# Kernel tuning notes

Hardware: AMD Instinct MI355X
Metric: run time of the kernel (lower is better)

The kernel has to match this reference:

```python
import jax, jax.numpy as jnp
import numpy as np

B, S, D = 2, 2048, 1024
H = 16
HD = D // H  # 64


def setup_inputs() -> dict:
    key = jax.random.key(0)
    ks = jax.random.split(key, 9)
    s = 1.0 / np.sqrt(D)
    x = jax.random.normal(ks[0], (B, S, D), dtype=jnp.float32)
    Wq = jax.random.normal(ks[1], (D, D), dtype=jnp.float32) * s
    Wk = jax.random.normal(ks[2], (D, D), dtype=jnp.float32) * s
    Wv = jax.random.normal(ks[3], (D, D), dtype=jnp.float32) * s
    Wo = jax.random.normal(ks[4], (D, D), dtype=jnp.float32) * s
    bq = jnp.zeros((D,), jnp.float32)
    bk = jnp.zeros((D,), jnp.float32)
    bv = jnp.zeros((D,), jnp.float32)
    bo = jnp.zeros((D,), jnp.float32)
    # causal mask, broadcastable to (B, H, S, S)
    mask = jnp.tril(jnp.ones((S, S), dtype=bool))[None, None, :, :]
    return {"x": x, "Wq": Wq, "bq": bq, "Wk": Wk, "bk": bk,
            "Wv": Wv, "bv": bv, "Wo": Wo, "bo": bo, "mask": mask}


def _split_heads(t):
    # (B, S, D) -> (B, H, S, HD)
    b, s, _ = t.shape
    return t.reshape(b, s, H, HD).transpose(0, 2, 1, 3)


def reference(x, Wq, bq, Wk, bk, Wv, bv, Wo, bo, mask):
    q = _split_heads(x @ Wq + bq)
    k = _split_heads(x @ Wk + bk)
    v = _split_heads(x @ Wv + bv)
    scale = 1.0 / jnp.sqrt(jnp.asarray(HD, dtype=q.dtype))
    scores = jnp.einsum('bhqd,bhkd->bhqk', q, k) * scale
    large_neg = jnp.finfo(scores.dtype).min
    scores = jnp.where(mask, scores, large_neg)
    attn = jax.nn.softmax(scores, axis=-1)
    out = jnp.einsum('bhqk,bhkd->bhqd', attn, v)  # (B,H,S,HD)
    out = out.transpose(0, 2, 1, 3).reshape(x.shape[0], x.shape[1], D)
    return out @ Wo + bo
```

## Files before the change

kernel.cpp:

```cpp
#include <hip/hip_runtime.h>
#include <hip/hip_bf16.h>

typedef __attribute__((ext_vector_type(8))) short bf16x8;
typedef __attribute__((ext_vector_type(4))) float f32x4;

#define B_DIM  2
#define S_DIM  2048
#define D_DIM  1024
#define H_DIM  16
#define HD_DIM 64

__device__ __forceinline__ float bf2f(ushort u) {
    union { unsigned int ui; float f; } c; c.ui = ((unsigned int)u) << 16; return c.f;
}
__device__ __forceinline__ ushort f2bf(float f) {
    __hip_bfloat16 h = __float2bfloat16(f);
    return *reinterpret_cast<ushort*>(&h);
}

__device__ __forceinline__ void async_cp16(const ushort* g, ushort* l) {
    __builtin_amdgcn_global_load_lds(
        (const __attribute__((address_space(1))) void*)g,
        (__attribute__((address_space(3))) void*)l, 16, 0, 0);
}

__global__ __launch_bounds__(256) void detect_kernel(const ushort* __restrict__ x,
                                                     int* __restrict__ flag) {
    __shared__ int any;
    int tid = threadIdx.x;
    if (tid == 0) any = 0;
    __syncthreads();
    int cnt = 0;
    for (int j = 0; j < 64; ++j) {
        ushort u = x[tid * 64 + j];
        if (((u >> 7) & 0xFF) == 0xFF) cnt++;
    }
    if (cnt) atomicOr(&any, 1);
    __syncthreads();
    if (tid == 0) *flag = any ? 1 : 0;
}

__global__ __launch_bounds__(256) void prep_kernel(const void* __restrict__ x,
                                                   const void* __restrict__ Wq,
                                                   const void* __restrict__ Wk,
                                                   const void* __restrict__ Wv,
                                                   const void* __restrict__ Wo,
                                                   const void* __restrict__ bq,
                                                   const void* __restrict__ bk,
                                                   const void* __restrict__ bv,
                                                   const void* __restrict__ bo,
                                                   ushort* __restrict__ xc,
                                                   ushort* __restrict__ Wqkvt,
                                                   ushort* __restrict__ Wot,
                                                   float* __restrict__ biasf,
                                                   const int* __restrict__ flag) {
    int tid = threadIdx.x;
    int z = blockIdx.z;
    bool isf32 = (*flag != 0);

    if (z == 4) {
        int t = (blockIdx.y * 16 + blockIdx.x) * 256 + tid;
#pragma unroll
        for (int c = 0; c < 8; ++c) {
            int i = t + c * 65536;
            if (isf32) {
                const float* s = (const float*)x;
                f32x4 a = *(const f32x4*)&s[(size_t)i * 8];
                f32x4 b = *(const f32x4*)&s[(size_t)i * 8 + 4];
                bf16x8 o;
                o[0] = f2bf(a.x); o[1] = f2bf(a.y); o[2] = f2bf(a.z); o[3] = f2bf(a.w);
                o[4] = f2bf(b.x); o[5] = f2bf(b.y); o[6] = f2bf(b.z); o[7] = f2bf(b.w);
                *(bf16x8*)&xc[(size_t)i * 8] = o;
            } else {
                *(bf16x8*)&xc[(size_t)i * 8] =
                    *(const bf16x8*)&((const ushort*)x)[(size_t)i * 8];
            }
        }
        return;
    }
    if (z == 5) {
        int bid = blockIdx.y * 16 + blockIdx.x;
        if (bid >= 16) return;
        int i = bid * 256 + tid;
        int w = i >> 10, j = i & 1023;
        const void* s = (w == 0) ? bq : (w == 1) ? bk : (w == 2) ? bv : bo;
        biasf[i] = isf32 ? ((const float*)s)[j] : bf2f(((const ushort*)s)[j]);
        return;
    }

    __shared__ ushort tile[64][72];
    const void* src = (z == 0) ? Wq : (z == 1) ? Wk : (z == 2) ? Wv : Wo;
    ushort* dst = (z < 3) ? (Wqkvt + (size_t)z * D_DIM * D_DIM) : Wot;
    int r0 = blockIdx.y * 64, c0 = blockIdx.x * 64;
#pragma unroll
    for (int p = 0; p < 2; ++p) {
        int r = p * 32 + (tid >> 3);
        int c = (tid & 7) * 8;
        if (isf32) {
            const float* s = (const float*)src;
            f32x4 a = *(const f32x4*)&s[(size_t)(r0 + r) * D_DIM + c0 + c];
            f32x4 b = *(const f32x4*)&s[(size_t)(r0 + r) * D_DIM + c0 + c + 4];
            tile[r][c + 0] = f2bf(a.x); tile[r][c + 1] = f2bf(a.y);
            tile[r][c + 2] = f2bf(a.z); tile[r][c + 3] = f2bf(a.w);
            tile[r][c + 4] = f2bf(b.x); tile[r][c + 5] = f2bf(b.y);
            tile[r][c + 6] = f2bf(b.z); tile[r][c + 7] = f2bf(b.w);
        } else {
            *(bf16x8*)&tile[r][c] =
                *(const bf16x8*)&((const ushort*)src)[(size_t)(r0 + r) * D_DIM + c0 + c];
        }
    }
    __syncthreads();
#pragma unroll
    for (int p = 0; p < 2; ++p) {
        int n  = p * 32 + (tid >> 3);
        int cc = (tid & 7) * 8;
        bf16x8 v;
#pragma unroll
        for (int e = 0; e < 8; ++e) v[e] = (short)tile[cc + e][n];
        *(bf16x8*)&dst[(size_t)(c0 + n) * D_DIM + r0 + cc] = v;
    }
}

__global__ __launch_bounds__(256) void gemm128_kernel(const ushort* __restrict__ A,
                                                      const ushort* __restrict__ Bt,
                                                      const float* __restrict__ bias,
                                                      ushort* __restrict__ qkout,
                                                      ushort* __restrict__ vtout) {
    __shared__ ushort As[128 * 64];
    __shared__ ushort Bs[128 * 64];
    int tid  = threadIdx.x;
    int wave = tid >> 6;
    int lane = tid & 63;
    int l16  = lane & 15;
    int quad = lane >> 4;
    int m0   = blockIdx.y * 128;
    int n0   = blockIdx.x * 128;
    int wm   = wave >> 1;
    int wn   = wave & 1;
    const int K = 1024;

    f32x4 acc[4][4];
#pragma unroll
    for (int i = 0; i < 4; ++i)
#pragma unroll
        for (int j = 0; j < 4; ++j) acc[i][j] = (f32x4){0.f, 0.f, 0.f, 0.f};

    int lrow = lane >> 3;
    int gcol = ((lane & 7) ^ lrow) * 8;
    int sw   = l16 & 7;

    for (int kt = 0; kt < 16; ++kt) {
        int k0 = kt * 64;
#pragma unroll
        for (int j = 0; j < 4; ++j) {
            int chunk = wave * 4 + j;
            int grow  = chunk * 8 + lrow;
            async_cp16(&A[(size_t)(m0 + grow) * K + k0 + gcol], &As[chunk * 512]);
            async_cp16(&Bt[(size_t)(n0 + grow) * K + k0 + gcol], &Bs[chunk * 512]);
        }
        __syncthreads();

#pragma unroll
        for (int kb = 0; kb < 2; ++kb) {
            bf16x8 af[4], bf[4];
#pragma unroll
            for (int i = 0; i < 4; ++i)
                af[i] = *(const bf16x8*)&As[(wm * 64 + i * 16 + l16) * 64 +
                                            (((kb * 4 + quad) ^ sw) << 3)];
#pragma unroll
            for (int j = 0; j < 4; ++j)
                bf[j] = *(const bf16x8*)&Bs[(wn * 64 + j * 16 + l16) * 64 +
                                            (((kb * 4 + quad) ^ sw) << 3)];
#pragma unroll
            for (int i = 0; i < 4; ++i)
#pragma unroll
                for (int j = 0; j < 4; ++j)
                    acc[i][j] = __builtin_amdgcn_mfma_f32_16x16x32_bf16(af[i], bf[j],
                                                                        acc[i][j], 0, 0, 0);
        }
        __syncthreads();
    }

    const size_t TSZ = (size_t)B_DIM * H_DIM * S_DIM * HD_DIM;
#pragma unroll
    for (int j = 0; j < 4; ++j) {
        int n = n0 + wn * 64 + j * 16 + l16;
        float bv = bias[n];
        int which = n >> 10;
        int n1 = n & 1023;
        int h = n1 >> 6, hd = n1 & 63;
#pragma unroll
        for (int i = 0; i < 4; ++i) {
            int mb = m0 + wm * 64 + i * 16 + quad * 4;
            int b = mb >> 11, s = mb & (S_DIM - 1);
            float v4[4];
#pragma unroll
            for (int r = 0; r < 4; ++r) v4[r] = acc[i][j][r] + bv;
            if (which == 2) {
                ushort pk[4];
#pragma unroll
                for (int r = 0; r < 4; ++r) pk[r] = f2bf(v4[r]);
                *(uint2*)&vtout[(((size_t)(b * H_DIM + h) * HD_DIM + hd)) * S_DIM + s] =
                    *(uint2*)pk;
            } else {
#pragma unroll
                for (int r = 0; r < 4; ++r) {
                    float v = v4[r];
                    if (which == 0) v *= 0.18033688011f;
                    qkout[which * TSZ +
                          ((((size_t)(b * H_DIM + h)) * S_DIM + s + r) << 6) + hd] = f2bf(v);
                }
            }
        }
    }
}

__global__ __launch_bounds__(256) void gemm64_kernel(const ushort* __restrict__ A,
                                                     const ushort* __restrict__ Bt,
                                                     const float* __restrict__ bias,
                                                     void* __restrict__ out,
                                                     const int* __restrict__ flag) {
    __shared__ ushort As[64 * 64];
    __shared__ ushort Bs[128 * 64];
    int tid  = threadIdx.x;
    int wave = tid >> 6;
    int lane = tid & 63;
    int l16  = lane & 15;
    int quad = lane >> 4;
    int m0   = blockIdx.y * 64;
    int n0   = blockIdx.x * 128;
    const int K = 1024;

    f32x4 acc[4][2];
#pragma unroll
    for (int i = 0; i < 4; ++i)
#pragma unroll
        for (int j = 0; j < 2; ++j) acc[i][j] = (f32x4){0.f, 0.f, 0.f, 0.f};

    int lrow = lane >> 3;
    int gcol = ((lane & 7) ^ lrow) * 8;
    int sw   = l16 & 7;

    for (int kt = 0; kt < 16; ++kt) {
        int k0 = kt * 64;
#pragma unroll
        for (int j = 0; j < 2; ++j) {
            int chunk = wave * 2 + j;
            int grow  = chunk * 8 + lrow;
            async_cp16(&A[(size_t)(m0 + grow) * K + k0 + gcol], &As[chunk * 512]);
        }
#pragma unroll
        for (int j = 0; j < 4; ++j) {
            int chunk = wave * 4 + j;
            int grow  = chunk * 8 + lrow;
            async_cp16(&Bt[(size_t)(n0 + grow) * K + k0 + gcol], &Bs[chunk * 512]);
        }
        __syncthreads();

#pragma unroll
        for (int kb = 0; kb < 2; ++kb) {
            bf16x8 af[4], bf[2];
#pragma unroll
            for (int i = 0; i < 4; ++i)
                af[i] = *(const bf16x8*)&As[(i * 16 + l16) * 64 +
                                            (((kb * 4 + quad) ^ sw) << 3)];
#pragma unroll
            for (int j = 0; j < 2; ++j)
                bf[j] = *(const bf16x8*)&Bs[(wave * 32 + j * 16 + l16) * 64 +
                                            (((kb * 4 + quad) ^ sw) << 3)];
#pragma unroll
            for (int i = 0; i < 4; ++i)
#pragma unroll
                for (int j = 0; j < 2; ++j)
                    acc[i][j] = __builtin_amdgcn_mfma_f32_16x16x32_bf16(af[i], bf[j],
                                                                        acc[i][j], 0, 0, 0);
        }
        __syncthreads();
    }

    int outf32 = *flag;
#pragma unroll
    for (int j = 0; j < 2; ++j) {
        int n = n0 + wave * 32 + j * 16 + l16;
        float bv = bias[n];
#pragma unroll
        for (int i = 0; i < 4; ++i)
#pragma unroll
            for (int r = 0; r < 4; ++r) {
                int m = m0 + i * 16 + quad * 4 + r;
                float v = acc[i][j][r] + bv;
                if (outf32) ((float*)out)[(size_t)m * D_DIM + n] = v;
                else        ((ushort*)out)[(size_t)m * D_DIM + n] = f2bf(v);
            }
    }
}

#define SLD 72
__global__ __launch_bounds__(256) void attn_kernel(const ushort* __restrict__ Qg,
                                                   const ushort* __restrict__ Kg,
                                                   const ushort* __restrict__ Vt,
                                                   ushort* __restrict__ attn_out) {
    __shared__ ushort Ks[64 * SLD];
    __shared__ ushort Vs[64 * SLD];
    __shared__ ushort Ss[64 * SLD];
    int tid  = threadIdx.x;
    int wave = tid >> 6;
    int lane = tid & 63;
    int l16  = lane & 15;
    int quad = lane >> 4;
    int bh   = blockIdx.x;
    int y    = blockIdx.y;
    int qt   = (y < 8) ? y : (y < 16) ? (23 - y) : (y < 24) ? y : (55 - y);
    int q0   = qt * 64;

    const ushort* Qb = Qg + (size_t)bh * S_DIM * HD_DIM;
    const ushort* Kb = Kg + (size_t)bh * S_DIM * HD_DIM;
    const ushort* Vb = Vt + (size_t)bh * HD_DIM * S_DIM;

    bf16x8 qf[2];
#pragma unroll
    for (int ks = 0; ks < 2; ++ks)
        qf[ks] = *(const bf16x8*)&Qb[(size_t)(q0 + wave * 16 + l16) * HD_DIM +
                                     ks * 32 + quad * 8];

    f32x4 o[4];
#pragma unroll
    for (int i = 0; i < 4; ++i) o[i] = (f32x4){0.f, 0.f, 0.f, 0.f};
    float rsum = 0.f;

    int srow = tid >> 3;
    int scol = (tid & 7) * 8;

    bf16x8 kr[2], vr[2];
#pragma unroll
    for (int p = 0; p < 2; ++p) {
        kr[p] = *(const bf16x8*)&Kb[(size_t)(srow + 32 * p) * HD_DIM + scol];
        vr[p] = *(const bf16x8*)&Vb[(size_t)(srow + 32 * p) * S_DIM + scol];
    }

    int ntiles = qt + 1;
    for (int t = 0; t < ntiles; ++t) {
        __syncthreads();
#pragma unroll
        for (int p = 0; p < 2; ++p) {
            *(bf16x8*)&Ks[(srow + 32 * p) * SLD + scol] = kr[p];
            *(bf16x8*)&Vs[(srow + 32 * p) * SLD + scol] = vr[p];
        }
        __syncthreads();
        if (t + 1 < ntiles) {
            int k1 = (t + 1) * 64;
#pragma unroll
            for (int p = 0; p < 2; ++p) {
                kr[p] = *(const bf16x8*)&Kb[(size_t)(k1 + srow + 32 * p) * HD_DIM + scol];
                vr[p] = *(const bf16x8*)&Vb[(size_t)(srow + 32 * p) * S_DIM + k1 + scol];
            }
        }

        int k0 = t * 64;

        f32x4 sc[4];
#pragma unroll
        for (int i = 0; i < 4; ++i) sc[i] = (f32x4){0.f, 0.f, 0.f, 0.f};
#pragma unroll
        for (int ks = 0; ks < 2; ++ks)
#pragma unroll
            for (int nb = 0; nb < 4; ++nb) {
                bf16x8 kf = *(const bf16x8*)&Ks[(nb * 16 + l16) * SLD + ks * 32 + quad * 8];
                sc[nb] = __builtin_amdgcn_mfma_f32_16x16x32_bf16(kf, qf[ks],
                                                                 sc[nb], 0, 0, 0);
            }

        if (t == ntiles - 1) {
            int qglob = q0 + wave * 16 + l16;
#pragma unroll
            for (int nb = 0; nb < 4; ++nb) {
                int key = k0 + nb * 16 + quad * 4;
#pragma unroll
                for (int r = 0; r < 4; ++r)
                    if (key + r > qglob) sc[nb][r] = -1e30f;
            }
        }

#pragma unroll
        for (int nb = 0; nb < 4; ++nb) {
            ushort pk[4];
            float ps = 0.f;
#pragma unroll
            for (int r = 0; r < 4; ++r) {
                float p = __builtin_amdgcn_exp2f(sc[nb][r]);
                ps += p;
                pk[r] = f2bf(p);
            }
            rsum += ps;
            *(uint2*)&Ss[(wave * 16 + l16) * SLD + nb * 16 + quad * 4] = *(uint2*)pk;
        }

        bf16x8 pf[2];
#pragma unroll
        for (int ks = 0; ks < 2; ++ks)
            pf[ks] = *(const bf16x8*)&Ss[(wave * 16 + l16) * SLD + ks * 32 + quad * 8];

#pragma unroll
        for (int ks = 0; ks < 2; ++ks)
#pragma unroll
            for (int nb = 0; nb < 4; ++nb) {
                bf16x8 vf = *(const bf16x8*)&Vs[(nb * 16 + l16) * SLD + ks * 32 + quad * 8];
                o[nb] = __builtin_amdgcn_mfma_f32_16x16x32_bf16(pf[ks], vf,
                                                                o[nb], 0, 0, 0);
            }
    }

    rsum += __shfl_xor(rsum, 16, 64);
    rsum += __shfl_xor(rsum, 32, 64);

    int b = bh >> 4, h = bh & 15;
    float inv[4];
#pragma unroll
    for (int r = 0; r < 4; ++r)
        inv[r] = 1.f / __shfl(rsum, quad * 4 + r, 64);
#pragma unroll
    for (int nb = 0; nb < 4; ++nb)
#pragma unroll
        for (int r = 0; r < 4; ++r) {
            int q = q0 + wave * 16 + quad * 4 + r;
            attn_out[(size_t)(b * S_DIM + q) * D_DIM + h * HD_DIM + nb * 16 + l16] =
                f2bf(o[nb][r] * inv[r]);
        }
}

extern "C" void kernel_launch(void* const* d_in, const int* in_sizes, int n_in,
                              void* d_out, int out_size, void* d_ws, size_t ws_size,
                              hipStream_t stream) {
    const void* x  = d_in[0];
    const void* Wq = d_in[1];
    const void* bq = d_in[2];
    const void* Wk = d_in[3];
    const void* bk = d_in[4];
    const void* Wv = d_in[5];
    const void* bv = d_in[6];
    const void* Wo = d_in[7];
    const void* bo = d_in[8];

    char* ws = (char*)d_ws;
    const size_t MB = 1024 * 1024;
    const size_t base = 64 * 1024;
    int*    flag   = (int*)ws;
    float*  biasf  = (float*)(ws + 4096);
    ushort* xc     = (ushort*)(ws + base);
    ushort* Wqkvt  = (ushort*)(ws + base + 8  * MB);
    ushort* Wot    = (ushort*)(ws + base + 14 * MB);
    ushort* Qc     = (ushort*)(ws + base + 16 * MB);
    ushort* Vtp    = (ushort*)(ws + base + 40 * MB);
    ushort* attn   = xc;

    dim3 tb(256);

    detect_kernel<<<1, tb, 0, stream>>>((const ushort*)x, flag);

    dim3 pg(16, 16, 6);
    prep_kernel<<<pg, tb, 0, stream>>>(x, Wq, Wk, Wv, Wo, bq, bk, bv, bo,
                                       xc, Wqkvt, Wot, biasf, flag);

    dim3 gq(3 * D_DIM / 128, (B_DIM * S_DIM) / 128);
    gemm128_kernel<<<gq, tb, 0, stream>>>(xc, Wqkvt, biasf, Qc, Vtp);

    dim3 ag(B_DIM * H_DIM, S_DIM / 64);
    attn_kernel<<<ag, tb, 0, stream>>>(Qc, Qc + (size_t)B_DIM * H_DIM * S_DIM * HD_DIM,
                                       Vtp, attn);

    dim3 go(D_DIM / 128, (B_DIM * S_DIM) / 64);
    gemm64_kernel<<<go, tb, 0, stream>>>(attn, Wot, biasf + 3072, d_out, flag);
}
```

Baseline: 195.6 us.

## Double-buffer attention K/V via async LDS loads and keep P in registers

The attention kernel now loads K and V tiles straight into double-buffered, XOR-swizzled shared memory with async global-to-LDS copies, replacing register staging and removing one barrier per tile. The softmax probabilities are packed to bf16 and rearranged across lanes with permlane swaps, so the P tile no longer goes through shared memory. It also adds setprio hints around the MFMA blocks and asks for 4 blocks per CU in the launch bounds. The risks are getting the lane-permutation layout wrong for the MFMA A operand, extra register pressure from holding the V fragments, and only one barrier guarding the buffer reuse.

```diff
diff --git a/kernel.cpp b/kernel.cpp
--- a/kernel.cpp
+++ b/kernel.cpp
@@ -22,6 +22,18 @@
     __builtin_amdgcn_global_load_lds(
         (const __attribute__((address_space(1))) void*)g,
         (__attribute__((address_space(3))) void*)l, 16, 0, 0);
+}
+
+__device__ __forceinline__ unsigned int cvt_pk_bf16(float lo, float hi) {
+    unsigned int d;
+    asm volatile("v_cvt_pk_bf16_f32 %0, %1, %2" : "=v"(d) : "v"(lo), "v"(hi));
+    return d;
+}
+__device__ __forceinline__ void pl32swap(unsigned int& a, unsigned int& b) {
+    asm volatile("v_permlane32_swap_b32 %0, %1" : "+v"(a), "+v"(b));
+}
+__device__ __forceinline__ void pl16swap(unsigned int& a, unsigned int& b) {
+    asm volatile("v_permlane16_swap_b32 %0, %1" : "+v"(a), "+v"(b));
 }
 
 __global__ __launch_bounds__(256) void detect_kernel(const ushort* __restrict__ x,
@@ -295,14 +307,12 @@
     }
 }
 
-#define SLD 72
-__global__ __launch_bounds__(256) void attn_kernel(const ushort* __restrict__ Qg,
-                                                   const ushort* __restrict__ Kg,
-                                                   const ushort* __restrict__ Vt,
-                                                   ushort* __restrict__ attn_out) {
-    __shared__ ushort Ks[64 * SLD];
-    __shared__ ushort Vs[64 * SLD];
-    __shared__ ushort Ss[64 * SLD];
+__global__ __launch_bounds__(256, 4) void attn_kernel(const ushort* __restrict__ Qg,
+                                                      const ushort* __restrict__ Kg,
+                                                      const ushort* __restrict__ Vt,
+                                                      ushort* __restrict__ attn_out) {
+    __shared__ ushort Ks[2][64 * 64];
+    __shared__ ushort Vs[2][64 * 64];
     int tid  = threadIdx.x;
     int wave = tid >> 6;
     int lane = tid & 63;
@@ -328,47 +338,58 @@
     for (int i = 0; i < 4; ++i) o[i] = (f32x4){0.f, 0.f, 0.f, 0.f};
     float rsum = 0.f;
 
-    int srow = tid >> 3;
-    int scol = (tid & 7) * 8;
-
-    bf16x8 kr[2], vr[2];
-#pragma unroll
-    for (int p = 0; p < 2; ++p) {
-        kr[p] = *(const bf16x8*)&Kb[(size_t)(srow + 32 * p) * HD_DIM + scol];
-        vr[p] = *(const bf16x8*)&Vb[(size_t)(srow + 32 * p) * S_DIM + scol];
+    int lrow = lane >> 3;
+    int gcol = ((lane & 7) ^ lrow) * 8;
+    int sw   = l16 & 7;
+
+#pragma unroll
+    for (int j = 0; j < 2; ++j) {
+        int chunk = wave * 2 + j;
+        int grow  = chunk * 8 + lrow;
+        async_cp16(&Kb[(size_t)grow * HD_DIM + gcol], &Ks[0][chunk * 512]);
+        async_cp16(&Vb[(size_t)grow * S_DIM + gcol], &Vs[0][chunk * 512]);
     }
 
     int ntiles = qt + 1;
+    int p = 0;
     for (int t = 0; t < ntiles; ++t) {
-        __syncthreads();
-#pragma unroll
-        for (int p = 0; p < 2; ++p) {
-            *(bf16x8*)&Ks[(srow + 32 * p) * SLD + scol] = kr[p];
-            *(bf16x8*)&Vs[(srow + 32 * p) * SLD + scol] = vr[p];
-        }
         __syncthreads();
         if (t + 1 < ntiles) {
             int k1 = (t + 1) * 64;
 #pragma unroll
-            for (int p = 0; p < 2; ++p) {
-                kr[p] = *(const bf16x8*)&Kb[(size_t)(k1 + srow + 32 * p) * HD_DIM + scol];
-                vr[p] = *(const bf16x8*)&Vb[(size_t)(srow + 32 * p) * S_DIM + k1 + scol];
+            for (int j = 0; j < 2; ++j) {
+                int chunk = wave * 2 + j;
+                int grow  = chunk * 8 + lrow;
+                async_cp16(&Kb[(size_t)(k1 + grow) * HD_DIM + gcol],
+                           &Ks[p ^ 1][chunk * 512]);
+                async_cp16(&Vb[(size_t)grow * S_DIM + k1 + gcol],
+                           &Vs[p ^ 1][chunk * 512]);
             }
         }
-
         int k0 = t * 64;
 
         f32x4 sc[4];
 #pragma unroll
         for (int i = 0; i < 4; ++i) sc[i] = (f32x4){0.f, 0.f, 0.f, 0.f};
+        __builtin_amdgcn_s_setprio(1);
 #pragma unroll
         for (int ks = 0; ks < 2; ++ks)
 #pragma unroll
             for (int nb = 0; nb < 4; ++nb) {
-                bf16x8 kf = *(const bf16x8*)&Ks[(nb * 16 + l16) * SLD + ks * 32 + quad * 8];
+                bf16x8 kf = *(const bf16x8*)&Ks[p][(nb * 16 + l16) * 64 +
+                                                   (((ks * 4 + quad) ^ sw) << 3)];
                 sc[nb] = __builtin_amdgcn_mfma_f32_16x16x32_bf16(kf, qf[ks],
                                                                  sc[nb], 0, 0, 0);
             }
+        __builtin_amdgcn_s_setprio(0);
+
+        bf16x8 vf[2][4];
+#pragma unroll
+        for (int ks = 0; ks < 2; ++ks)
+#pragma unroll
+            for (int nb = 0; nb < 4; ++nb)
+                vf[ks][nb] = *(const bf16x8*)&Vs[p][(nb * 16 + l16) * 64 +
+                                                    (((ks * 4 + quad) ^ sw) << 3)];
 
         if (t == ntiles - 1) {
             int qglob = q0 + wave * 16 + l16;
@@ -381,33 +402,45 @@
             }
         }
 
+        unsigned int W[4][2];
+        float psn[4];
 #pragma unroll
         for (int nb = 0; nb < 4; ++nb) {
-            ushort pk[4];
-            float ps = 0.f;
-#pragma unroll
-            for (int r = 0; r < 4; ++r) {
-                float p = __builtin_amdgcn_exp2f(sc[nb][r]);
-                ps += p;
-                pk[r] = f2bf(p);
-            }
-            rsum += ps;
-            *(uint2*)&Ss[(wave * 16 + l16) * SLD + nb * 16 + quad * 4] = *(uint2*)pk;
-        }
-
+            float pv[4];
+#pragma unroll
+            for (int r = 0; r < 4; ++r) pv[r] = __builtin_amdgcn_exp2f(sc[nb][r]);
+            psn[nb] = (pv[0] + pv[1]) + (pv[2] + pv[3]);
+            W[nb][0] = cvt_pk_bf16(pv[0], pv[1]);
+            W[nb][1] = cvt_pk_bf16(pv[2], pv[3]);
+        }
+        rsum += (psn[0] + psn[1]) + (psn[2] + psn[3]);
+
+#pragma unroll
+        for (int pp = 0; pp < 2; ++pp) {
+            pl32swap(W[0][pp], W[1][pp]);
+            pl32swap(W[2][pp], W[3][pp]);
+            pl16swap(W[0][pp], W[1][pp]);
+            pl16swap(W[2][pp], W[3][pp]);
+        }
         bf16x8 pf[2];
+        {
+            union { unsigned int u[4]; bf16x8 v; } c0, c1;
+            c0.u[0] = W[0][0]; c0.u[1] = W[0][1];
+            c0.u[2] = W[1][0]; c0.u[3] = W[1][1];
+            c1.u[0] = W[2][0]; c1.u[1] = W[2][1];
+            c1.u[2] = W[3][0]; c1.u[3] = W[3][1];
+            pf[0] = c0.v; pf[1] = c1.v;
+        }
+
+        __builtin_amdgcn_s_setprio(1);
 #pragma unroll
         for (int ks = 0; ks < 2; ++ks)
-            pf[ks] = *(const bf16x8*)&Ss[(wave * 16 + l16) * SLD + ks * 32 + quad * 8];
-
-#pragma unroll
-        for (int ks = 0; ks < 2; ++ks)
-#pragma unroll
-            for (int nb = 0; nb < 4; ++nb) {
-                bf16x8 vf = *(const bf16x8*)&Vs[(nb * 16 + l16) * SLD + ks * 32 + quad * 8];
-                o[nb] = __builtin_amdgcn_mfma_f32_16x16x32_bf16(pf[ks], vf,
+#pragma unroll
+            for (int nb = 0; nb < 4; ++nb)
+                o[nb] = __builtin_amdgcn_mfma_f32_16x16x32_bf16(pf[ks], vf[ks][nb],
                                                                 o[nb], 0, 0, 0);
-            }
+        __builtin_amdgcn_s_setprio(0);
+        p ^= 1;
     }
 
     rsum += __shfl_xor(rsum, 16, 64);
```

Measured after the change: 195.2 us. No clear change (-0.2%).
